# Optimization experiments

Hardware: AMD Instinct MI355X
Metric: run time of the kernel (lower is better)

Reference implementation:

```python
import jax, jax.numpy as jnp
import numpy as np

TWO_PI = 2.0 * np.pi


def setup_inputs() -> dict:
    key = jax.random.key(0)
    k1, k2 = jax.random.split(key)
    B, S, F, U = 16, 1024, 2048, 2048
    x = jax.random.normal(k1, (B, S, F), dtype=jnp.float32)
    # Dense(quantum_projection): weight [2F, U], bias [U]
    W = jax.random.normal(k2, (2 * F, U), dtype=jnp.float32) * (1.0 / np.sqrt(2 * F))
    b = jnp.zeros((U,), dtype=jnp.float32)
    return {"x": x, "W": W, "b": b}


def reference(x, W, b):
    # x: [B, S, F]
    qp = x * TWO_PI                                   # quantum_params
    quantum_enhanced = jnp.tanh(qp) + 0.1 * (jnp.sin(qp) * jnp.cos(qp * 0.5))
    # diag(outer(v, v)) == v**2 -- skip the O(F^2) matmul
    entanglement = quantum_enhanced * quantum_enhanced
    feats = jnp.concatenate([quantum_enhanced, entanglement], axis=-1)  # [B,S,2F]
    out = jnp.tanh(jnp.einsum('bsf,fu->bsu', feats, W) + b)             # [B,S,U]
    return out
```

## Files before the change

### kernel.cpp

```cpp
#include <hip/hip_runtime.h>
#include <hip/hip_bf16.h>
#include <math.h>


typedef __bf16 b16x8 __attribute__((ext_vector_type(8)));
typedef float f32x4 __attribute__((ext_vector_type(4)));

constexpr int Mdim = 16384;
constexpr int Fdim = 2048;
constexpr int Kdim = 4096;
constexpr int Ndim = 2048;

__device__ __forceinline__ float tanh_2pix(float x) {
  float ax = fabsf(x);
  float e = __expf(-12.566370614359172f * ax);
  float t = (1.0f - e) * __builtin_amdgcn_rcpf(1.0f + e);
  return copysignf(t, x);
}

__device__ __forceinline__ float fast_tanh(float x) {
  float ax = fabsf(x);
  float e = __expf(-2.0f * ax);
  float t = (1.0f - e) * __builtin_amdgcn_rcpf(1.0f + e);
  return copysignf(t, x);
}

struct __align__(16) B8 { __bf16 v[8]; };

__global__ void feats_kernel(const float* __restrict__ x, __bf16* __restrict__ feats) {
  int idx = blockIdx.x * blockDim.x + threadIdx.x;
  long i8 = (long)idx << 3;
  float4 xv0 = reinterpret_cast<const float4*>(x)[idx * 2];
  float4 xv1 = reinterpret_cast<const float4*>(x)[idx * 2 + 1];
  float q[8] = {xv0.x, xv0.y, xv0.z, xv0.w, xv1.x, xv1.y, xv1.z, xv1.w};
  B8 qe, en;
#pragma unroll
  for (int j = 0; j < 8; ++j) {
    float xx = q[j];
    float s = __builtin_amdgcn_sinf(xx);
    float c = __builtin_amdgcn_cosf(0.5f * xx);
    float v = tanh_2pix(xx) + 0.1f * s * c;
    qe.v[j] = (__bf16)v;
    en.v[j] = (__bf16)(v * v);
  }
  int m = (int)(i8 >> 11);
  int f = (int)(i8 & (Fdim - 1));
  size_t base = (size_t)m * Kdim + f;
  *reinterpret_cast<B8*>(feats + base) = qe;
  *reinterpret_cast<B8*>(feats + base + Fdim) = en;
}

__global__ void wtrans_kernel(const float* __restrict__ W, __bf16* __restrict__ Wt) {
  __shared__ float tile[32][33];
  int bn = blockIdx.x;
  int bk = blockIdx.y;
  int tx = threadIdx.x;
  int ty = threadIdx.y;
#pragma unroll
  for (int i = 0; i < 4; ++i) {
    int kk = bk * 32 + ty + i * 8;
    tile[ty + i * 8][tx] = W[(size_t)kk * Ndim + bn * 32 + tx];
  }
  __syncthreads();
#pragma unroll
  for (int i = 0; i < 4; ++i) {
    int nn = bn * 32 + ty + i * 8;
    Wt[(size_t)nn * Kdim + bk * 32 + tx] = (__bf16)tile[tx][ty + i * 8];
  }
}

typedef const __attribute__((address_space(1))) void* gptr1;
typedef __attribute__((address_space(3))) void* lptr3;

__device__ __forceinline__ void gld_lds16(const __bf16* g, __bf16* l) {
  __builtin_amdgcn_global_load_lds((gptr1)g, (lptr3)l, 16, 0, 0);
}

#define BARRIER()    asm volatile("s_barrier" ::: "memory")
#define WAIT_LGKM0() asm volatile("s_waitcnt lgkmcnt(0)" ::: "memory")
#define WAIT_VM(n)   asm volatile("s_waitcnt vmcnt(" #n ")" ::: "memory")

#define TILE(h, S1, S2, S3, S4) do {                                        \
    const int s0_ = (h) & 3, s1_ = ((h) + 1) & 3;                           \
    rdA(s0_, 0); rdB(s0_);                                                  \
    if (S1) stageA((h) + 3);                                                \
    BARRIER(); WAIT_LGKM0();                                                \
    mfma4(0);                                                               \
    BARRIER();                                                              \
    rdA(s0_, 4);                                                            \
    if (S2) stageB((h) + 4);                                                \
    BARRIER(); WAIT_LGKM0();                                                \
    mfma4(4);                                                               \
    BARRIER();                                                              \
    rdA(s1_, 0); rdB(s1_);                                                  \
    if (S3) stageA((h) + 4);                                                \
    BARRIER(); WAIT_LGKM0();                                                \
    mfma4(0);                                                               \
    BARRIER();                                                              \
    rdA(s1_, 4);                                                            \
    if (S4) stageB((h) + 5);                                                \
    BARRIER(); WAIT_LGKM0();                                                \
    mfma4(4);                                                               \
  } while (0)

__global__ __launch_bounds__(512, 2) void gemm_tanh_kernel(
    const __bf16* __restrict__ A,
    const __bf16* __restrict__ Bt,
    const float* __restrict__ bias,
    float* __restrict__ out) {
  __shared__ __align__(16) __bf16 smem[65536];
  __bf16* const sA = smem;
  __bf16* const sB = smem + 32768;

  const int tid = threadIdx.x;
  const int wv = tid >> 6;
  const int lane = tid & 63;

  const int orig = blockIdx.y * 8 + blockIdx.x;
  const int wg = (orig & 7) * 64 + (orig >> 3);
  const int m0 = (wg >> 3) * 256;
  const int n0 = (wg & 7) * 256;

  const int wm = (wv >> 2) * 128;
  const int wn = (wv & 3) * 64;
  const int lr = lane & 15;
  const int lq = lane >> 4;

  const int L0 = wv * 128 + lane;
  const int L1 = L0 + 64;
  const int r0 = L0 >> 2, r1 = L1 >> 2;
  const int c0 = (L0 & 3) ^ ((r0 >> 1) & 3);
  const int c1 = (L1 & 3) ^ ((r1 >> 1) & 3);
  const __bf16* gA0 = A + (size_t)(m0 + r0) * Kdim + c0 * 8;
  const __bf16* gA1 = A + (size_t)(m0 + r1) * Kdim + c1 * 8;
  const __bf16* gB0 = Bt + (size_t)(n0 + r0) * Kdim + c0 * 8;
  const __bf16* gB1 = Bt + (size_t)(n0 + r1) * Kdim + c1 * 8;
  const int d0 = wv * 1024;
  const int d1 = d0 + 512;

  auto stageA = [&](int h) {
    __bf16* s = sA + (h & 3) * 8192;
    gld_lds16(gA0 + h * 32, s + d0);
    gld_lds16(gA1 + h * 32, s + d1);
  };
  auto stageB = [&](int h) {
    __bf16* s = sB + (h & 3) * 8192;
    gld_lds16(gB0 + h * 32, s + d0);
    gld_lds16(gB1 + h * 32, s + d1);
  };

  const int chunk = (lq ^ ((lr >> 1) & 3)) * 8;
  const int ard = (wm + lr) * 32 + chunk;
  const int brd = (wn + lr) * 32 + chunk;

  f32x4 acc[8][4];
#pragma unroll
  for (int i = 0; i < 8; ++i)
#pragma unroll
    for (int j = 0; j < 4; ++j) acc[i][j] = (f32x4){0.f, 0.f, 0.f, 0.f};

  b16x8 av[4], bv[4];
  auto rdA = [&](int s, int fb) {
#pragma unroll
    for (int i = 0; i < 4; ++i)
      av[i] = *reinterpret_cast<const b16x8*>(sA + s * 8192 + ard + (fb + i) * 512);
  };
  auto rdB = [&](int s) {
#pragma unroll
    for (int i = 0; i < 4; ++i)
      bv[i] = *reinterpret_cast<const b16x8*>(sB + s * 8192 + brd + i * 512);
  };
  auto mfma4 = [&](int fb) {
    __builtin_amdgcn_s_setprio(1);
#pragma unroll
    for (int i = 0; i < 4; ++i)
#pragma unroll
      for (int j = 0; j < 4; ++j)
        acc[fb + i][j] =
            __builtin_amdgcn_mfma_f32_16x16x32_bf16(av[i], bv[j], acc[fb + i][j], 0, 0, 0);
    __builtin_amdgcn_s_setprio(0);
  };

  float bval[4];
#pragma unroll
  for (int j = 0; j < 4; ++j) bval[j] = bias[n0 + wn + j * 16 + lr];
  WAIT_VM(0);

  stageA(0); stageB(0); stageA(1); stageB(1);
  WAIT_VM(4);
  stageA(2); stageB(2); stageB(3);
  WAIT_VM(6);
  BARRIER();

  for (int u = 0; u < 31; ++u) {
    const int h = u * 4;
    TILE(h, 1, 1, 1, 1);
    WAIT_VM(6); BARRIER();
    TILE(h + 2, 1, 1, 1, 1);
    WAIT_VM(6); BARRIER();
  }
  TILE(124, 1, 0, 0, 0);
  WAIT_VM(0); BARRIER();
  TILE(126, 0, 0, 0, 0);

#pragma unroll
  for (int j = 0; j < 4; ++j) {
    const int gn = n0 + wn + j * 16 + lr;
#pragma unroll
    for (int i = 0; i < 8; ++i) {
      const int gm = m0 + wm + i * 16 + lq * 4;
#pragma unroll
      for (int r = 0; r < 4; ++r) {
        float v = acc[i][j][r] + bval[j];
        out[(size_t)(gm + r) * Ndim + gn] = fast_tanh(v);
      }
    }
  }
}

extern "C" void kernel_launch(void* const* d_in, const int* in_sizes, int n_in,
                              void* d_out, int out_size, void* d_ws, size_t ws_size,
                              hipStream_t stream) {
  const float* x = (const float*)d_in[0];
  const float* W = (const float*)d_in[1];
  const float* b = (const float*)d_in[2];
  float* out = (float*)d_out;

  __bf16* Wt = (__bf16*)d_ws;
  __bf16* feats = Wt + (size_t)Ndim * Kdim;

  hipLaunchKernelGGL(feats_kernel, dim3(Mdim * Fdim / 8 / 256), dim3(256), 0,
                     stream, x, feats);
  hipLaunchKernelGGL(wtrans_kernel, dim3(Ndim / 32, Kdim / 32), dim3(32, 8), 0,
                     stream, W, Wt);
  hipLaunchKernelGGL(gemm_tanh_kernel, dim3(Ndim / 256, Mdim / 256), dim3(512),
                     0, stream, feats, Wt, b, out);
}
```

Measured before the change: 495.0 us.

## Double-buffer LDS fragment registers to overlap reads with MFMA

Replaces the single set of A/B register fragments with two ping-pong sets, so LDS reads for the next sub-step are issued right after the current MFMA batch instead of before it. The number of barriers per sub-step drops from two to one, and waits on LDS reads are deferred until just before the fragments are needed. The cost is more vector registers per thread, which could cause spills or lower occupancy under the 512x2 launch bounds. The reworked staging order and vmcnt waits in the tail also risk reading LDS slots before they are fully written.

```diff
diff --git a/kernel.cpp b/kernel.cpp
--- a/kernel.cpp
+++ b/kernel.cpp
@@ -80,27 +80,15 @@
 #define WAIT_LGKM0() asm volatile("s_waitcnt lgkmcnt(0)" ::: "memory")
 #define WAIT_VM(n)   asm volatile("s_waitcnt vmcnt(" #n ")" ::: "memory")
 
-#define TILE(h, S1, S2, S3, S4) do {                                        \
-    const int s0_ = (h) & 3, s1_ = ((h) + 1) & 3;                           \
-    rdA(s0_, 0); rdB(s0_);                                                  \
-    if (S1) stageA((h) + 3);                                                \
-    BARRIER(); WAIT_LGKM0();                                                \
-    mfma4(0);                                                               \
-    BARRIER();                                                              \
-    rdA(s0_, 4);                                                            \
-    if (S2) stageB((h) + 4);                                                \
-    BARRIER(); WAIT_LGKM0();                                                \
-    mfma4(4);                                                               \
-    BARRIER();                                                              \
-    rdA(s1_, 0); rdB(s1_);                                                  \
-    if (S3) stageA((h) + 4);                                                \
-    BARRIER(); WAIT_LGKM0();                                                \
-    mfma4(0);                                                               \
-    BARRIER();                                                              \
-    rdA(s1_, 4);                                                            \
-    if (S4) stageB((h) + 5);                                                \
-    BARRIER(); WAIT_LGKM0();                                                \
-    mfma4(4);                                                               \
+#define MFMA16(AV, BV, FB) do {                                               \
+    __builtin_amdgcn_s_setprio(1);                                            \
+    _Pragma("unroll")                                                         \
+    for (int i_ = 0; i_ < 4; ++i_)                                            \
+      _Pragma("unroll")                                                       \
+      for (int j_ = 0; j_ < 4; ++j_)                                          \
+        acc[(FB) + i_][j_] = __builtin_amdgcn_mfma_f32_16x16x32_bf16(         \
+            AV[i_], BV[j_], acc[(FB) + i_][j_], 0, 0, 0);                     \
+    __builtin_amdgcn_s_setprio(0);                                            \
   } while (0)
 
 __global__ __launch_bounds__(512, 2) void gemm_tanh_kernel(
@@ -159,26 +147,16 @@
 #pragma unroll
     for (int j = 0; j < 4; ++j) acc[i][j] = (f32x4){0.f, 0.f, 0.f, 0.f};
 
-  b16x8 av[4], bv[4];
-  auto rdA = [&](int s, int fb) {
+  b16x8 av0[4], av1[4], bv0[4], bv1[4];
+  auto rdA = [&](b16x8 (&dst)[4], int slot, int fb) {
 #pragma unroll
     for (int i = 0; i < 4; ++i)
-      av[i] = *reinterpret_cast<const b16x8*>(sA + s * 8192 + ard + (fb + i) * 512);
-  };
-  auto rdB = [&](int s) {
+      dst[i] = *reinterpret_cast<const b16x8*>(sA + slot * 8192 + ard + (fb + i) * 512);
+  };
+  auto rdB = [&](b16x8 (&dst)[4], int slot) {
 #pragma unroll
     for (int i = 0; i < 4; ++i)
-      bv[i] = *reinterpret_cast<const b16x8*>(sB + s * 8192 + brd + i * 512);
-  };
-  auto mfma4 = [&](int fb) {
-    __builtin_amdgcn_s_setprio(1);
-#pragma unroll
-    for (int i = 0; i < 4; ++i)
-#pragma unroll
-      for (int j = 0; j < 4; ++j)
-        acc[fb + i][j] =
-            __builtin_amdgcn_mfma_f32_16x16x32_bf16(av[i], bv[j], acc[fb + i][j], 0, 0, 0);
-    __builtin_amdgcn_s_setprio(0);
+      dst[i] = *reinterpret_cast<const b16x8*>(sB + slot * 8192 + brd + i * 512);
   };
 
   float bval[4];
@@ -191,17 +169,44 @@
   stageA(2); stageB(2); stageB(3);
   WAIT_VM(6);
   BARRIER();
+  rdA(av0, 0, 0); rdB(bv0, 0);
 
   for (int u = 0; u < 31; ++u) {
     const int h = u * 4;
-    TILE(h, 1, 1, 1, 1);
-    WAIT_VM(6); BARRIER();
-    TILE(h + 2, 1, 1, 1, 1);
-    WAIT_VM(6); BARRIER();
-  }
-  TILE(124, 1, 0, 0, 0);
-  WAIT_VM(0); BARRIER();
-  TILE(126, 0, 0, 0, 0);
+    WAIT_LGKM0();              BARRIER(); stageA(h + 3);
+    MFMA16(av0, bv0, 0);       rdA(av1, 0, 4);
+    WAIT_LGKM0(); WAIT_VM(6);  BARRIER(); stageB(h + 4);
+    MFMA16(av1, bv0, 4);       rdA(av0, 1, 0); rdB(bv1, 1);
+    WAIT_LGKM0();              BARRIER(); stageA(h + 4);
+    MFMA16(av0, bv1, 0);       rdA(av1, 1, 4);
+    WAIT_LGKM0(); WAIT_VM(6);  BARRIER(); stageB(h + 5);
+    MFMA16(av1, bv1, 4);       rdA(av0, 2, 0); rdB(bv0, 2);
+    WAIT_LGKM0();              BARRIER(); stageA(h + 5);
+    MFMA16(av0, bv0, 0);       rdA(av1, 2, 4);
+    WAIT_LGKM0(); WAIT_VM(6);  BARRIER(); stageB(h + 6);
+    MFMA16(av1, bv0, 4);       rdA(av0, 3, 0); rdB(bv1, 3);
+    WAIT_LGKM0();              BARRIER(); stageA(h + 6);
+    MFMA16(av0, bv1, 0);       rdA(av1, 3, 4);
+    WAIT_LGKM0(); WAIT_VM(6);  BARRIER(); stageB(h + 7);
+    MFMA16(av1, bv1, 4);       rdA(av0, 0, 0); rdB(bv0, 0);
+  }
+
+  WAIT_LGKM0();              BARRIER(); stageA(127);
+  MFMA16(av0, bv0, 0);       rdA(av1, 0, 4);
+  WAIT_LGKM0(); WAIT_VM(6);  BARRIER();
+  MFMA16(av1, bv0, 4);       rdA(av0, 1, 0); rdB(bv1, 1);
+  WAIT_LGKM0();              BARRIER();
+  MFMA16(av0, bv1, 0);       rdA(av1, 1, 4);
+  WAIT_LGKM0(); WAIT_VM(4);  BARRIER();
+  MFMA16(av1, bv1, 4);       rdA(av0, 2, 0); rdB(bv0, 2);
+  WAIT_LGKM0();              BARRIER();
+  MFMA16(av0, bv0, 0);       rdA(av1, 2, 4);
+  WAIT_LGKM0(); WAIT_VM(0);  BARRIER();
+  MFMA16(av1, bv0, 4);       rdA(av0, 3, 0); rdB(bv1, 3);
+  WAIT_LGKM0();              BARRIER();
+  MFMA16(av0, bv1, 0);       rdA(av1, 3, 4);
+  WAIT_LGKM0();
+  MFMA16(av1, bv1, 4);
 
 #pragma unroll
   for (int j = 0; j < 4; ++j) {
```

After: 487.9 us. About the same (-1.4%).
